# Kernel optimization log

Hardware: AMD Instinct MI355X
Metric: run time of the kernel (lower is better)

Reference implementation:

```python
import jax, jax.numpy as jnp
import numpy as np

B, T, D = 4, 2048, 1024
H = 16
HD = D // H  # 64


def setup_inputs() -> dict:
    key = jax.random.key(0)
    ks = jax.random.split(key, 5)
    scale = 0.02
    x = jax.random.normal(ks[0], (B, T, D), dtype=jnp.float32)
    W_qkv = jax.random.normal(ks[1], (D, 3 * D), dtype=jnp.float32) * scale
    b_qkv = jnp.zeros((3 * D,), dtype=jnp.float32)
    W_proj = jax.random.normal(ks[2], (D, D), dtype=jnp.float32) * scale
    b_proj = jnp.zeros((D,), dtype=jnp.float32)
    return {"x": x, "W_qkv": W_qkv, "b_qkv": b_qkv, "W_proj": W_proj, "b_proj": b_proj}


def reference(x, W_qkv, b_qkv, W_proj, b_proj):
    b, t, c = x.shape
    qkv = x @ W_qkv + b_qkv  # [b, t, 3c]
    q, k, v = jnp.split(qkv, 3, axis=-1)
    # [b, h, t, hd]
    q = q.reshape(b, t, H, HD).transpose(0, 2, 1, 3)
    k = k.reshape(b, t, H, HD).transpose(0, 2, 1, 3)
    v = v.reshape(b, t, H, HD).transpose(0, 2, 1, 3)
    att = jnp.einsum('bhqd,bhkd->bhqk', q, k) / jnp.sqrt(jnp.float32(HD))
    causal = jnp.tril(jnp.ones((t, t), dtype=bool))
    att = jnp.where(causal[None, None], att, jnp.float32(-jnp.inf))
    att = jax.nn.softmax(att, axis=-1)
    y = jnp.einsum('bhqk,bhkd->bhqd', att, v)
    y = y.transpose(0, 2, 1, 3).reshape(b, t, c)
    return y @ W_proj + b_proj
```

## Files before the change

kernel.cpp:

```cpp
#include <hip/hip_runtime.h>
#include <hip/hip_bf16.h>
#include <cmath>
#include <cstdint>

#define B_ 4
#define T_ 2048
#define D_ 1024
#define H_ 16
#define HD_ 64
#define M_ (B_*T_)
#define NQKV_ 3072

#define SCALE_Q 0.18033688011112042f

typedef float f32x4 __attribute__((ext_vector_type(4)));
typedef float f32x16 __attribute__((ext_vector_type(16)));
typedef __bf16 bf16x8 __attribute__((ext_vector_type(8)));
typedef __bf16 bf16x4 __attribute__((ext_vector_type(4)));

#define MFMA16(a, b, c) __builtin_amdgcn_mfma_f32_16x16x32_bf16((a), (b), (c), 0, 0, 0)
#define MFMA32(a, b, c) __builtin_amdgcn_mfma_f32_32x32x16_bf16((a), (b), (c), 0, 0, 0)

#if defined(__has_builtin)
#if __has_builtin(__builtin_amdgcn_global_load_lds)
#define HAVE_GLDS 1
#endif
#endif

#ifdef HAVE_GLDS
#define GLDS16(g, l) __builtin_amdgcn_global_load_lds( \
    (const __attribute__((address_space(1))) void*)(g), \
    (__attribute__((address_space(3))) void*)(l), 16, 0, 0)
#endif

__device__ inline float hexp2(float x) {
  float r; asm("v_exp_f32 %0, %1" : "=v"(r) : "v"(x)); return r;
}

__device__ inline uint32_t pack2bf(float a, float b) {
  union { __bf16 h[2]; uint32_t u; } x;
  x.h[0] = (__bf16)a; x.h[1] = (__bf16)b;
  return x.u;
}

__global__ __launch_bounds__(256) void k_cvt_bf16(const float4* __restrict__ in,
                                                  bf16x4* __restrict__ out, int n4) {
  int i = blockIdx.x * 256 + threadIdx.x;
  if (i >= n4) return;
  float4 v = in[i];
  bf16x4 o;
  o[0] = (__bf16)v.x; o[1] = (__bf16)v.y; o[2] = (__bf16)v.z; o[3] = (__bf16)v.w;
  out[i] = o;
}

__global__ __launch_bounds__(256) void k_transpose_cvt(const float* __restrict__ in,
                                                       __bf16* __restrict__ out,
                                                       int R, int C) {
  __shared__ float tile[64][65];
  int r0 = blockIdx.y * 64, c0 = blockIdx.x * 64;
#pragma unroll
  for (int i = 0; i < 16; ++i) {
    int e = threadIdx.x + i * 256;
    int lr = e >> 6, lc = e & 63;
    tile[lr][lc] = in[(size_t)(r0 + lr) * C + c0 + lc];
  }
  __syncthreads();
#pragma unroll
  for (int i = 0; i < 16; ++i) {
    int e = threadIdx.x + i * 256;
    int lc = e >> 6, lr = e & 63;
    out[(size_t)(c0 + lc) * R + r0 + lr] = (__bf16)tile[lr][lc];
  }
}

__global__ __launch_bounds__(512) void k_gemm256(const __bf16* __restrict__ A,
                                                 const __bf16* __restrict__ Bt,
                                                 const float* __restrict__ bias,
                                                 __bf16* __restrict__ Qb,
                                                 __bf16* __restrict__ Kb,
                                                 __bf16* __restrict__ Vt) {
  __shared__ __bf16 lA[256 * 32];
  __shared__ __bf16 lB[128 * 32];
  const int tid = threadIdx.x;
  const int lane = tid & 63, w = tid >> 6;
  const int wr = w >> 1, wc = w & 1;
  const int r15 = lane & 15, rg = lane >> 4;
  const int mb = blockIdx.y, nb = blockIdx.x;
  const int K = D_;
  const int nk = K >> 5;

  const f32x4 zero = {0.f, 0.f, 0.f, 0.f};
  f32x4 acc[4][4];
#pragma unroll
  for (int m = 0; m < 4; ++m)
#pragma unroll
    for (int n = 0; n < 4; ++n) acc[m][n] = zero;

  const int cA0 = tid, cA1 = tid + 512;
  const int rowA0 = cA0 >> 2, rowA1 = cA1 >> 2, offA = (tid & 3) * 8;
  const int rowB = tid >> 2;
  const __bf16* Ab = A + (size_t)(mb * 256) * K;
  const __bf16* Bb = Bt + (size_t)(nb * 128) * K;

  for (int kb = 0; kb < nk; ++kb) {
    __syncthreads();
#ifdef HAVE_GLDS
    GLDS16(Ab + (size_t)rowA0 * K + kb * 32 + offA, &lA[cA0 * 8]);
    GLDS16(Ab + (size_t)rowA1 * K + kb * 32 + offA, &lA[cA1 * 8]);
    GLDS16(Bb + (size_t)rowB * K + kb * 32 + offA, &lB[tid * 8]);
#else
    {
      bf16x8 ta0 = *(const bf16x8*)(Ab + (size_t)rowA0 * K + kb * 32 + offA);
      bf16x8 ta1 = *(const bf16x8*)(Ab + (size_t)rowA1 * K + kb * 32 + offA);
      bf16x8 tb0 = *(const bf16x8*)(Bb + (size_t)rowB * K + kb * 32 + offA);
      *(bf16x8*)(&lA[cA0 * 8]) = ta0;
      *(bf16x8*)(&lA[cA1 * 8]) = ta1;
      *(bf16x8*)(&lB[tid * 8]) = tb0;
    }
#endif
    __syncthreads();
    bf16x8 af[4], bfr[4];
#pragma unroll
    for (int m = 0; m < 4; ++m)
      af[m] = *(const bf16x8*)(&lA[(wr * 64 + m * 16 + r15) * 32 + rg * 8]);
#pragma unroll
    for (int n = 0; n < 4; ++n)
      bfr[n] = *(const bf16x8*)(&lB[(wc * 64 + n * 16 + r15) * 32 + rg * 8]);
#pragma unroll
    for (int m = 0; m < 4; ++m)
#pragma unroll
      for (int n = 0; n < 4; ++n)
        acc[m][n] = MFMA16(af[m], bfr[n], acc[m][n]);
  }

  const int row0 = mb * 256 + wr * 64;
  const int col0 = nb * 128 + wc * 64;
#pragma unroll
  for (int m = 0; m < 4; ++m) {
#pragma unroll
    for (int n = 0; n < 4; ++n) {
      const int c = col0 + n * 16 + r15;
      const int r0 = row0 + m * 16 + rg * 4;
      const int which = c >> 10, cc = c & 1023;
      const int b = r0 >> 11, t0 = r0 & 2047;
      float v[4];
#pragma unroll
      for (int j = 0; j < 4; ++j) v[j] = acc[m][n][j] + bias[c];
      if (which == 0) {
        int hh = cc >> 6, hd = cc & 63;
#pragma unroll
        for (int j = 0; j < 4; ++j)
          Qb[((size_t)(b * H_ + hh) * T_ + t0 + j) * HD_ + hd] = (__bf16)(v[j] * SCALE_Q);
      } else if (which == 1) {
        int hh = cc >> 6, hd = cc & 63;
#pragma unroll
        for (int j = 0; j < 4; ++j)
          Kb[((size_t)(b * H_ + hh) * T_ + t0 + j) * HD_ + hd] = (__bf16)v[j];
      } else {
        int hh = cc >> 6, hd = cc & 63;
        bf16x4 pk;
#pragma unroll
        for (int j = 0; j < 4; ++j) pk[j] = (__bf16)v[j];
        *(bf16x4*)(Vt + ((size_t)(b * H_ + hh) * HD_ + hd) * T_ + t0) = pk;
      }
    }
  }
}

__global__ __launch_bounds__(256) void k_gemm_proj(const __bf16* __restrict__ A,
                                                   const __bf16* __restrict__ Bt,
                                                   const float* __restrict__ bias,
                                                   float* __restrict__ Cf,
                                                   int K, int N) {
  __shared__ __bf16 lA[128 * 32];
  __shared__ __bf16 lB[128 * 32];
  const int tid = threadIdx.x;
  const int lane = tid & 63, w = tid >> 6;
  const int wr = w >> 1, wc = w & 1;
  const int r15 = lane & 15, rg = lane >> 4;
  const int mb = blockIdx.y, nb = blockIdx.x;
  const int nk = K >> 5;

  const f32x4 zero = {0.f, 0.f, 0.f, 0.f};
  f32x4 acc[4][4];
#pragma unroll
  for (int m = 0; m < 4; ++m)
#pragma unroll
    for (int n = 0; n < 4; ++n) acc[m][n] = zero;

  const int c0 = tid, c1 = tid + 256;
  const int rowA0 = c0 >> 2, offA0 = (c0 & 3) * 8;
  const int rowA1 = c1 >> 2, offA1 = (c1 & 3) * 8;
  const __bf16* Ab = A + (size_t)(mb * 128) * K;
  const __bf16* Bb = Bt + (size_t)(nb * 128) * K;

  for (int kb = 0; kb < nk; ++kb) {
    __syncthreads();
#ifdef HAVE_GLDS
    GLDS16(Ab + (size_t)rowA0 * K + kb * 32 + offA0, &lA[c0 * 8]);
    GLDS16(Ab + (size_t)rowA1 * K + kb * 32 + offA1, &lA[c1 * 8]);
    GLDS16(Bb + (size_t)rowA0 * K + kb * 32 + offA0, &lB[c0 * 8]);
    GLDS16(Bb + (size_t)rowA1 * K + kb * 32 + offA1, &lB[c1 * 8]);
#else
    {
      bf16x8 ta0 = *(const bf16x8*)(Ab + (size_t)rowA0 * K + kb * 32 + offA0);
      bf16x8 ta1 = *(const bf16x8*)(Ab + (size_t)rowA1 * K + kb * 32 + offA1);
      bf16x8 tb0 = *(const bf16x8*)(Bb + (size_t)rowA0 * K + kb * 32 + offA0);
      bf16x8 tb1 = *(const bf16x8*)(Bb + (size_t)rowA1 * K + kb * 32 + offA1);
      *(bf16x8*)(&lA[c0 * 8]) = ta0;
      *(bf16x8*)(&lA[c1 * 8]) = ta1;
      *(bf16x8*)(&lB[c0 * 8]) = tb0;
      *(bf16x8*)(&lB[c1 * 8]) = tb1;
    }
#endif
    __syncthreads();
    bf16x8 af[4], bfr[4];
#pragma unroll
    for (int m = 0; m < 4; ++m)
      af[m] = *(const bf16x8*)(&lA[(wr * 64 + m * 16 + r15) * 32 + rg * 8]);
#pragma unroll
    for (int n = 0; n < 4; ++n)
      bfr[n] = *(const bf16x8*)(&lB[(wc * 64 + n * 16 + r15) * 32 + rg * 8]);
#pragma unroll
    for (int m = 0; m < 4; ++m)
#pragma unroll
      for (int n = 0; n < 4; ++n)
        acc[m][n] = MFMA16(af[m], bfr[n], acc[m][n]);
  }

  const int row0 = mb * 128 + wr * 64;
  const int col0 = nb * 128 + wc * 64;
#pragma unroll
  for (int m = 0; m < 4; ++m)
#pragma unroll
    for (int n = 0; n < 4; ++n)
#pragma unroll
      for (int j = 0; j < 4; ++j) {
        int r = row0 + m * 16 + rg * 4 + j;
        int c = col0 + n * 16 + r15;
        Cf[(size_t)r * N + c] = acc[m][n][j] + bias[c];
      }
}

__global__ __launch_bounds__(256) void k_attn(const __bf16* __restrict__ Qb,
                                              const __bf16* __restrict__ Kb,
                                              const __bf16* __restrict__ Vt,
                                              __bf16* __restrict__ Obuf) {
  __shared__ __bf16 lK[2][64 * 64];
  __shared__ __bf16 lV[2][64 * 64];
  const int tid = threadIdx.x;
  const int lane = tid & 63, w = tid >> 6;
  const int l31 = lane & 31, hi = lane >> 5;
  const int bh = blockIdx.y;
  const int b = bh >> 4, h = bh & 15;
  const __bf16* Qh = Qb + (size_t)bh * T_ * HD_;
  const __bf16* Kh = Kb + (size_t)bh * T_ * HD_;
  const __bf16* Vh = Vt + (size_t)bh * HD_ * T_;

  const int sRow0 = tid >> 3, sSw0 = (((tid) & 7) ^ (sRow0 & 7)) * 8;
  const int c1s = tid + 256;
  const int sRow1 = c1s >> 3, sSw1 = ((c1s & 7) ^ (sRow1 & 7)) * 8;

  auto STAGE = [&](int bufi, int kv0) {
#ifdef HAVE_GLDS
    GLDS16(Kh + (size_t)(kv0 + sRow0) * HD_ + sSw0, &lK[bufi][tid * 8]);
    GLDS16(Kh + (size_t)(kv0 + sRow1) * HD_ + sSw1, &lK[bufi][(tid + 256) * 8]);
    GLDS16(Vh + (size_t)sRow0 * T_ + kv0 + sSw0, &lV[bufi][tid * 8]);
    GLDS16(Vh + (size_t)sRow1 * T_ + kv0 + sSw1, &lV[bufi][(tid + 256) * 8]);
#else
    bf16x8 k0 = *(const bf16x8*)(Kh + (size_t)(kv0 + sRow0) * HD_ + sSw0);
    bf16x8 k1 = *(const bf16x8*)(Kh + (size_t)(kv0 + sRow1) * HD_ + sSw1);
    bf16x8 v0 = *(const bf16x8*)(Vh + (size_t)sRow0 * T_ + kv0 + sSw0);
    bf16x8 v1 = *(const bf16x8*)(Vh + (size_t)sRow1 * T_ + kv0 + sSw1);
    *(bf16x8*)(&lK[bufi][tid * 8]) = k0;
    *(bf16x8*)(&lK[bufi][(tid + 256) * 8]) = k1;
    *(bf16x8*)(&lV[bufi][tid * 8]) = v0;
    *(bf16x8*)(&lV[bufi][(tid + 256) * 8]) = v1;
#endif
  };

  int buf = 0;
  STAGE(0, 0);

  auto process_half = [&](int s, int nst, bool hasNext) {
    const int q0w = s * 128 + w * 32;
    bf16x8 qf[4];
#pragma unroll
    for (int ks = 0; ks < 4; ++ks)
      qf[ks] = *(const bf16x8*)(Qh + (size_t)(q0w + l31) * HD_ + ks * 16 + hi * 8);

    f32x16 o0, o1;
#pragma unroll
    for (int i = 0; i < 16; ++i) { o0[i] = 0.f; o1[i] = 0.f; }
    float lpart = 0.f;

    for (int i = 0; i < nst; ++i) {
      const int kv0 = i * 64;
      if (i + 1 < nst) STAGE(buf ^ 1, (i + 1) * 64);
      else if (hasNext) STAGE(buf ^ 1, 0);

      if (kv0 <= q0w + 31) {
        const bool masked = (kv0 + 63) > q0w;
        bf16x8 kf[2][4];
#pragma unroll
        for (int seg = 0; seg < 2; ++seg)
#pragma unroll
          for (int ks = 0; ks < 4; ++ks)
            kf[seg][ks] = *(const bf16x8*)(&lK[buf][(seg * 32 + l31) * 64 +
                                                   (((ks * 2 + hi) ^ (l31 & 7)) * 8)]);
        f32x16 s0, s1;
#pragma unroll
        for (int r = 0; r < 16; ++r) { s0[r] = 0.f; s1[r] = 0.f; }
        __builtin_amdgcn_s_setprio(1);
#pragma unroll
        for (int ks = 0; ks < 4; ++ks) s0 = MFMA32(kf[0][ks], qf[ks], s0);
#pragma unroll
        for (int ks = 0; ks < 4; ++ks) s1 = MFMA32(kf[1][ks], qf[ks], s1);
        __builtin_amdgcn_s_setprio(0);

        if (masked) {
#pragma unroll
          for (int r = 0; r < 16; ++r) {
            int rr = (r & 3) + 8 * (r >> 2) + 4 * hi;
            if (kv0 + rr > q0w + l31) s0[r] = -INFINITY;
            if (kv0 + 32 + rr > q0w + l31) s1[r] = -INFINITY;
          }
        }
        float rs = 0.f;
#pragma unroll
        for (int r = 0; r < 16; ++r) {
          s0[r] = hexp2(s0[r]); s1[r] = hexp2(s1[r]);
          rs += s0[r] + s1[r];
        }
        lpart += rs;

        bf16x8 vf[2][4];
#pragma unroll
        for (int dh = 0; dh < 2; ++dh)
#pragma unroll
          for (int ks = 0; ks < 4; ++ks)
            vf[dh][ks] = *(const bf16x8*)(&lV[buf][(dh * 32 + l31) * 64 +
                                                   (((ks * 2 + hi) ^ (l31 & 7)) * 8)]);

#pragma unroll
        for (int ks = 0; ks < 4; ++ks) {
          const f32x16& sv = (ks < 2) ? s0 : s1;
          const int off = (ks & 1) * 8;
          uint32_t w0 = pack2bf(sv[off + 0], sv[off + 1]);
          uint32_t w1 = pack2bf(sv[off + 2], sv[off + 3]);
          uint32_t w2 = pack2bf(sv[off + 4], sv[off + 5]);
          uint32_t w3 = pack2bf(sv[off + 6], sv[off + 7]);
          uint32_t sx = hi ? w0 : w2;
          uint32_t sy = hi ? w1 : w3;
          uint32_t px = (uint32_t)__shfl_xor((int)sx, 32, 64);
          uint32_t py = (uint32_t)__shfl_xor((int)sy, 32, 64);
          union { uint32_t u[4]; bf16x8 v; } pa;
          pa.u[0] = hi ? px : w0;
          pa.u[1] = hi ? py : w1;
          pa.u[2] = hi ? w2 : px;
          pa.u[3] = hi ? w3 : py;
          __builtin_amdgcn_s_setprio(1);
          o0 = MFMA32(pa.v, vf[0][ks], o0);
          o1 = MFMA32(pa.v, vf[1][ks], o1);
          __builtin_amdgcn_s_setprio(0);
        }
      }
      __syncthreads();
      buf ^= 1;
    }

    float lrun = lpart + __shfl_xor(lpart, 32, 64);
#pragma unroll
    for (int r = 0; r < 16; ++r) {
      int rr = (r & 3) + 8 * (r >> 2) + 4 * hi;
      float inv = 1.0f / __shfl(lrun, rr, 64);
      int row = q0w + rr;
      __bf16* op = Obuf + (size_t)(b * T_ + row) * D_ + h * HD_ + l31;
      op[0]  = (__bf16)(o0[r] * inv);
      op[32] = (__bf16)(o1[r] * inv);
    }
  };

  const int sA = 15 - blockIdx.x;
  const int sB = blockIdx.x;
  __syncthreads();
  process_half(sA, 2 * sA + 2, true);
  process_half(sB, 2 * sB + 2, false);
}

extern "C" void kernel_launch(void* const* d_in, const int* in_sizes, int n_in,
                              void* d_out, int out_size, void* d_ws, size_t ws_size,
                              hipStream_t stream) {
  const float* x      = (const float*)d_in[0];
  const float* W_qkv  = (const float*)d_in[1];
  const float* b_qkv  = (const float*)d_in[2];
  const float* W_proj = (const float*)d_in[3];
  const float* b_proj = (const float*)d_in[4];
  float* out = (float*)d_out;

  char* ws = (char*)d_ws;
  size_t o = 0;
  __bf16* xb     = (__bf16*)(ws + o); o += (size_t)M_ * D_ * 2;
  __bf16* wqkvt  = (__bf16*)(ws + o); o += (size_t)NQKV_ * D_ * 2;
  __bf16* wprojt = (__bf16*)(ws + o); o += (size_t)D_ * D_ * 2;
  __bf16* Qb     = (__bf16*)(ws + o); o += (size_t)M_ * D_ * 2;
  __bf16* Kb     = (__bf16*)(ws + o); o += (size_t)M_ * D_ * 2;
  __bf16* Vt     = (__bf16*)(ws + o); o += (size_t)M_ * D_ * 2;
  __bf16* Obuf   = (__bf16*)(ws + o); o += (size_t)M_ * D_ * 2;
  (void)ws_size; (void)in_sizes; (void)n_in; (void)out_size;

  k_cvt_bf16<<<(M_ * D_ / 4 + 255) / 256, 256, 0, stream>>>((const float4*)x, (bf16x4*)xb, M_ * D_ / 4);
  k_transpose_cvt<<<dim3(NQKV_ / 64, D_ / 64), 256, 0, stream>>>(W_qkv, wqkvt, D_, NQKV_);
  k_transpose_cvt<<<dim3(D_ / 64, D_ / 64), 256, 0, stream>>>(W_proj, wprojt, D_, D_);
  k_gemm256<<<dim3(NQKV_ / 128, M_ / 256), 512, 0, stream>>>(xb, wqkvt, b_qkv, Qb, Kb, Vt);
  k_attn<<<dim3(8, B_ * H_), 256, 0, stream>>>(Qb, Kb, Vt, Obuf);
  k_gemm_proj<<<dim3(D_ / 128, M_ / 128), 256, 0, stream>>>(Obuf, wprojt, b_proj, out, D_, D_);
}
```

Measured before the change: 197.5 us.

## Deepen QKV GEMM K-tile to 64 with XOR-swizzled LDS and use permlane32_swap

```diff
diff --git a/kernel.cpp b/kernel.cpp
--- a/kernel.cpp
+++ b/kernel.cpp
@@ -24,6 +24,9 @@
 #if defined(__has_builtin)
 #if __has_builtin(__builtin_amdgcn_global_load_lds)
 #define HAVE_GLDS 1
+#endif
+#if __has_builtin(__builtin_amdgcn_permlane32_swap)
+#define HAVE_PLSWAP 1
 #endif
 #endif
 
@@ -79,15 +82,15 @@
                                                  __bf16* __restrict__ Qb,
                                                  __bf16* __restrict__ Kb,
                                                  __bf16* __restrict__ Vt) {
-  __shared__ __bf16 lA[256 * 32];
-  __shared__ __bf16 lB[128 * 32];
+  __shared__ __bf16 lA[256 * 64];
+  __shared__ __bf16 lB[128 * 64];
   const int tid = threadIdx.x;
   const int lane = tid & 63, w = tid >> 6;
   const int wr = w >> 1, wc = w & 1;
   const int r15 = lane & 15, rg = lane >> 4;
   const int mb = blockIdx.y, nb = blockIdx.x;
   const int K = D_;
-  const int nk = K >> 5;
+  const int nt = K >> 6;
 
   const f32x4 zero = {0.f, 0.f, 0.f, 0.f};
   f32x4 acc[4][4];
@@ -96,41 +99,55 @@
 #pragma unroll
     for (int n = 0; n < 4; ++n) acc[m][n] = zero;
 
-  const int cA0 = tid, cA1 = tid + 512;
-  const int rowA0 = cA0 >> 2, rowA1 = cA1 >> 2, offA = (tid & 3) * 8;
-  const int rowB = tid >> 2;
   const __bf16* Ab = A + (size_t)(mb * 256) * K;
   const __bf16* Bb = Bt + (size_t)(nb * 128) * K;
 
-  for (int kb = 0; kb < nk; ++kb) {
+  for (int t = 0; t < nt; ++t) {
     __syncthreads();
+#pragma unroll
+    for (int i = 0; i < 4; ++i) {
+      const int c = tid + i * 512;
+      const int rA = c >> 3, g = (c & 7) ^ (rA & 7);
 #ifdef HAVE_GLDS
-    GLDS16(Ab + (size_t)rowA0 * K + kb * 32 + offA, &lA[cA0 * 8]);
-    GLDS16(Ab + (size_t)rowA1 * K + kb * 32 + offA, &lA[cA1 * 8]);
-    GLDS16(Bb + (size_t)rowB * K + kb * 32 + offA, &lB[tid * 8]);
+      GLDS16(Ab + (size_t)rA * K + t * 64 + g * 8, &lA[c * 8]);
 #else
-    {
-      bf16x8 ta0 = *(const bf16x8*)(Ab + (size_t)rowA0 * K + kb * 32 + offA);
-      bf16x8 ta1 = *(const bf16x8*)(Ab + (size_t)rowA1 * K + kb * 32 + offA);
-      bf16x8 tb0 = *(const bf16x8*)(Bb + (size_t)rowB * K + kb * 32 + offA);
-      *(bf16x8*)(&lA[cA0 * 8]) = ta0;
-      *(bf16x8*)(&lA[cA1 * 8]) = ta1;
-      *(bf16x8*)(&lB[tid * 8]) = tb0;
-    }
-#endif
+      bf16x8 v = *(const bf16x8*)(Ab + (size_t)rA * K + t * 64 + g * 8);
+      *(bf16x8*)(&lA[c * 8]) = v;
+#endif
+    }
+#pragma unroll
+    for (int i = 0; i < 2; ++i) {
+      const int c = tid + i * 512;
+      const int rB = c >> 3, g = (c & 7) ^ (rB & 7);
+#ifdef HAVE_GLDS
+      GLDS16(Bb + (size_t)rB * K + t * 64 + g * 8, &lB[c * 8]);
+#else
+      bf16x8 v = *(const bf16x8*)(Bb + (size_t)rB * K + t * 64 + g * 8);
+      *(bf16x8*)(&lB[c * 8]) = v;
+#endif
+    }
     __syncthreads();
-    bf16x8 af[4], bfr[4];
-#pragma unroll
-    for (int m = 0; m < 4; ++m)
-      af[m] = *(const bf16x8*)(&lA[(wr * 64 + m * 16 + r15) * 32 + rg * 8]);
-#pragma unroll
-    for (int n = 0; n < 4; ++n)
-      bfr[n] = *(const bf16x8*)(&lB[(wc * 64 + n * 16 + r15) * 32 + rg * 8]);
-#pragma unroll
-    for (int m = 0; m < 4; ++m)
-#pragma unroll
-      for (int n = 0; n < 4; ++n)
-        acc[m][n] = MFMA16(af[m], bfr[n], acc[m][n]);
+#pragma unroll
+    for (int ksub = 0; ksub < 2; ++ksub) {
+      bf16x8 af[4], bfr[4];
+#pragma unroll
+      for (int m = 0; m < 4; ++m) {
+        const int row = wr * 64 + m * 16 + r15;
+        const int cc = (ksub * 4 + rg) ^ (r15 & 7);
+        af[m] = *(const bf16x8*)(&lA[(row * 8 + cc) * 8]);
+      }
+#pragma unroll
+      for (int n = 0; n < 4; ++n) {
+        const int row = wc * 64 + n * 16 + r15;
+        const int cc = (ksub * 4 + rg) ^ (r15 & 7);
+        bfr[n] = *(const bf16x8*)(&lB[(row * 8 + cc) * 8]);
+      }
+#pragma unroll
+      for (int m = 0; m < 4; ++m)
+#pragma unroll
+        for (int n = 0; n < 4; ++n)
+          acc[m][n] = MFMA16(af[m], bfr[n], acc[m][n]);
+    }
   }
 
   const int row0 = mb * 256 + wr * 64;
@@ -350,15 +367,24 @@
           uint32_t w1 = pack2bf(sv[off + 2], sv[off + 3]);
           uint32_t w2 = pack2bf(sv[off + 4], sv[off + 5]);
           uint32_t w3 = pack2bf(sv[off + 6], sv[off + 7]);
+          union { uint32_t u[4]; bf16x8 v; } pa;
+#ifdef HAVE_PLSWAP
+          auto rA = __builtin_amdgcn_permlane32_swap((int)w0, (int)w2, false, false);
+          auto rB = __builtin_amdgcn_permlane32_swap((int)w1, (int)w3, false, false);
+          pa.u[0] = (uint32_t)rA[0];
+          pa.u[1] = (uint32_t)rB[0];
+          pa.u[2] = (uint32_t)rA[1];
+          pa.u[3] = (uint32_t)rB[1];
+#else
           uint32_t sx = hi ? w0 : w2;
           uint32_t sy = hi ? w1 : w3;
           uint32_t px = (uint32_t)__shfl_xor((int)sx, 32, 64);
           uint32_t py = (uint32_t)__shfl_xor((int)sy, 32, 64);
-          union { uint32_t u[4]; bf16x8 v; } pa;
           pa.u[0] = hi ? px : w0;
           pa.u[1] = hi ? py : w1;
           pa.u[2] = hi ? w2 : px;
           pa.u[3] = hi ? w3 : py;
+#endif
           __builtin_amdgcn_s_setprio(1);
           o0 = MFMA32(pa.v, vf[0][ks], o0);
           o1 = MFMA32(pa.v, vf[1][ks], o1);
```

After: 190.9 us. -3.4%, faster.
